# Kernel tuning notes

Hardware: AMD Instinct MI355X
Metric: run time of the kernel (lower is better)

## Reference

```python
import math
import jax, jax.numpy as jnp
import numpy as np

NUM_HEADS = 16
WINDOW = 64  # neighbor_size
NEG_INF = -1e30


def setup_inputs() -> dict:
    key = jax.random.key(0)
    ks = jax.random.split(key, 5)
    B, L, D = 2, 2048, 1024
    x = jax.random.normal(ks[0], (B, L, D), dtype=jnp.float32)
    s = 0.02
    Wq = jax.random.normal(ks[1], (D, D), dtype=jnp.float32) * s
    Wk = jax.random.normal(ks[2], (D, D), dtype=jnp.float32) * s
    Wv = jax.random.normal(ks[3], (D, D), dtype=jnp.float32) * s
    Wo = jax.random.normal(ks[4], (D, D), dtype=jnp.float32) * s
    return {
        "x": x, "Wq": Wq, "Wk": Wk, "Wv": Wv, "Wo": Wo,
        "sep_gate": jnp.float32(0.1),
        "align_gate": jnp.float32(0.1),
        "coh_gate": jnp.float32(0.1),
    }


def reference(x, Wq, Wk, Wv, Wo, sep_gate, align_gate, coh_gate):
    B, L, D = x.shape
    H = NUM_HEADS
    hd = D // H
    scale = math.sqrt(hd)

    # projections (torch Linear: y = x @ W.T), split heads -> (B, H, L, hd)
    def proj(W):
        return (x @ W.T).reshape(B, L, H, hd).transpose(0, 2, 1, 3)

    q, k, v = proj(Wq), proj(Wk), proj(Wv)

    # raw scores (B, H, L, L)
    scores = jnp.einsum("bhqd,bhkd->bhqk", q, k) / scale

    # Reynolds rules (applied BEFORE masking, mean over full kv dim, as in source)
    similarity = jax.nn.sigmoid(scores)
    separation = -sep_gate * similarity ** 2
    alignment = align_gate * scores
    score_mean = jnp.mean(scores, axis=-1, keepdims=True)
    cohesion = -coh_gate * jnp.abs(scores - score_mean)
    scores = scores + separation + alignment + cohesion

    # causal sliding-window mask: attend iff 0 <= i - j < WINDOW
    i = jnp.arange(L)[:, None]
    j = jnp.arange(L)[None, :]
    dist = i - j
    masked = (dist < 0) | (dist >= WINDOW)  # (L, L) True = blocked
    scores = jnp.where(masked[None, None, :, :], NEG_INF, scores)

    attn = jax.nn.softmax(scores, axis=-1)  # dropout p=0.0 -> identity
    out = jnp.einsum("bhqk,bhkd->bhqd", attn, v)
    out = out.transpose(0, 2, 1, 3).reshape(B, L, D)
    return out @ Wo.T
```

## Files before the change

### kernel.cpp

```cpp
#include <hip/hip_runtime.h>
#include <math.h>

#define L_SEQ 2048
#define DMODEL 1024
#define HEADS 16
#define HD 64
#define BATCH 2
#define MROWS (BATCH*L_SEQ)
#define KDIM 1024

typedef short bfrag8 __attribute__((ext_vector_type(8)));
typedef float f32x4f __attribute__((ext_vector_type(4)));

__device__ __forceinline__ unsigned short f2bf(float f) {
    unsigned u = __float_as_uint(f);
    unsigned r = u + 0x7FFFu + ((u >> 16) & 1u);
    return (unsigned short)(r >> 16);
}
__device__ __forceinline__ float bf2f(unsigned short h) {
    return __uint_as_float(((unsigned)h) << 16);
}

__global__ __launch_bounds__(256) void convert_bf16(
    const float* __restrict__ x, const float* __restrict__ wq,
    const float* __restrict__ wk, const float* __restrict__ wv,
    const float* __restrict__ wo,
    unsigned short* __restrict__ xb, unsigned short* __restrict__ qwb,
    unsigned short* __restrict__ kwb, unsigned short* __restrict__ vwb,
    unsigned short* __restrict__ owb)
{
    const int bid = blockIdx.x;
    const float* src; unsigned short* dst; size_t base;
    if (bid < 4096) { src = x; dst = xb; base = (size_t)bid * 1024; }
    else {
        const int r = bid - 4096; const int w = r >> 10; const int off = r & 1023;
        src = (w==0) ? wq : (w==1) ? wk : (w==2) ? wv : wo;
        dst = (w==0) ? qwb : (w==1) ? kwb : (w==2) ? vwb : owb;
        base = (size_t)off * 1024;
    }
    const size_t idx = base + (size_t)threadIdx.x * 4;
    float4 v = *(const float4*)&src[idx];
    ushort4 o;
    o.x = f2bf(v.x); o.y = f2bf(v.y); o.z = f2bf(v.z); o.w = f2bf(v.w);
    *(ushort4*)&dst[idx] = o;
}

#define GBK 32

template<int MODE>
__global__ void mfma_gemm(
    const unsigned short* __restrict__ A,
    const unsigned short* __restrict__ W0, const unsigned short* __restrict__ W1,
    const unsigned short* __restrict__ W2,
    void* __restrict__ C0v, void* __restrict__ C1v, void* __restrict__ C2v)
{
    __shared__ short As[128*GBK];
    __shared__ short Bs[128*GBK];

    const int tid  = threadIdx.x;
    const int wave = tid >> 6, lane = tid & 63;
    const int m0   = blockIdx.x * 128;
    const int n0g  = blockIdx.y * 128;

    const unsigned short* Wp; int n0; int which = 0;
    if (MODE == 1) {
        which = n0g >> 10;
        n0 = n0g & 1023;
        Wp = (which==0) ? W0 : (which==1) ? W1 : W2;
    } else { n0 = n0g; Wp = W0; }

    const int quad = lane >> 4, lm = lane & 15;
    const int wm = wave >> 1, wn = wave & 1;

    f32x4f acc[4][4] = {};

    const int ebase0 = wave * 1024;

    for (int k0 = 0; k0 < KDIM; k0 += GBK) {
        __syncthreads();
        #pragma unroll
        for (int i = 0; i < 2; ++i) {
            const int ebase = ebase0 + i * 512;
            const int e = ebase + lane * 8;
            const int row = e >> 5, col = e & 31;
            __builtin_amdgcn_global_load_lds(
                (const __attribute__((address_space(1))) void*)(A + (size_t)(m0 + row) * KDIM + k0 + col),
                (__attribute__((address_space(3))) void*)(&As[ebase]), 16, 0, 0);
            __builtin_amdgcn_global_load_lds(
                (const __attribute__((address_space(1))) void*)(Wp + (size_t)(n0 + row) * KDIM + k0 + col),
                (__attribute__((address_space(3))) void*)(&Bs[ebase]), 16, 0, 0);
        }
        __syncthreads();

        bfrag8 af[4], bf[4];
        #pragma unroll
        for (int t = 0; t < 4; ++t) {
            af[t] = *(const bfrag8*)&As[(wm*64 + t*16 + lm)*GBK + quad*8];
            bf[t] = *(const bfrag8*)&Bs[(wn*64 + t*16 + lm)*GBK + quad*8];
        }
        #pragma unroll
        for (int mt = 0; mt < 4; ++mt)
            #pragma unroll
            for (int nt = 0; nt < 4; ++nt)
                acc[mt][nt] = __builtin_amdgcn_mfma_f32_16x16x32_bf16(
                    af[mt], bf[nt], acc[mt][nt], 0, 0, 0);
    }

    if (MODE == 1) {
        unsigned short* Cp = (unsigned short*)((which==0) ? C0v : (which==1) ? C1v : C2v);
        #pragma unroll
        for (int mt = 0; mt < 4; ++mt)
            #pragma unroll
            for (int nt = 0; nt < 4; ++nt) {
                const int gn = n0 + wn*64 + nt*16 + lm;
                const int h = gn >> 6, d = gn & 63;
                #pragma unroll
                for (int r = 0; r < 4; ++r) {
                    const int gm = m0 + wm*64 + mt*16 + quad*4 + r;
                    const int b = gm >> 11, l = gm & (L_SEQ-1);
                    Cp[(((size_t)(b*HEADS + h) * L_SEQ) + l) * HD + d] = f2bf(acc[mt][nt][r]);
                }
            }
    } else {
        float* Cp = (float*)C0v;
        #pragma unroll
        for (int mt = 0; mt < 4; ++mt)
            #pragma unroll
            for (int nt = 0; nt < 4; ++nt) {
                const int gn = n0 + wn*64 + nt*16 + lm;
                #pragma unroll
                for (int r = 0; r < 4; ++r) {
                    const int gm = m0 + wm*64 + mt*16 + quad*4 + r;
                    Cp[(size_t)gm * DMODEL + gn] = acc[mt][nt][r];
                }
            }
    }
}

__global__ __launch_bounds__(256) void kmean_from_k(
    const unsigned short* __restrict__ kb, float* __restrict__ kmean)
{
    __shared__ float part[4][64];
    const int bh = blockIdx.x, t = threadIdx.x;
    const int d = t & 63, seg = t >> 6;
    const unsigned short* kp = kb + ((size_t)bh * L_SEQ + seg * 512) * HD + d;
    float s0 = 0.f, s1 = 0.f, s2 = 0.f, s3 = 0.f;
    #pragma unroll 4
    for (int l = 0; l < 512; l += 4) {
        s0 += bf2f(kp[(size_t)(l+0) * HD]);
        s1 += bf2f(kp[(size_t)(l+1) * HD]);
        s2 += bf2f(kp[(size_t)(l+2) * HD]);
        s3 += bf2f(kp[(size_t)(l+3) * HD]);
    }
    part[seg][d] = (s0 + s1) + (s2 + s3);
    __syncthreads();
    if (t < 64)
        kmean[bh * HD + t] = (part[0][t] + part[1][t] + part[2][t] + part[3][t])
                             * (1.f / (float)L_SEQ);
}

#define QT 64
#define KROWS 128
#define VROWS 144
#define KS_STRIDE 72
#define VT_STRIDE 152
#define P_STRIDE 104

__global__ __launch_bounds__(256, 3) void attn_kernel(
    const unsigned short* __restrict__ qb, const unsigned short* __restrict__ kb,
    const unsigned short* __restrict__ vb, const float* __restrict__ kmean,
    const float* __restrict__ g_sep, const float* __restrict__ g_align,
    const float* __restrict__ g_coh, unsigned short* __restrict__ out)
{
    __shared__ unsigned short ks[KROWS * KS_STRIDE];
    __shared__ unsigned short vst[HD * VT_STRIDE];
    __shared__ unsigned short pl[QT * P_STRIDE];
    __shared__ float smean[QT];
    __shared__ float km_s[HD];

    const int tid = threadIdx.x;
    const int bh = blockIdx.x >> 5;
    const int qt = blockIdx.x & 31;
    const int q0 = qt * QT;
    const int j0 = q0 - 63;

    const unsigned short* kbh = kb + (size_t)bh * L_SEQ * HD;
    const unsigned short* vbh = vb + (size_t)bh * L_SEQ * HD;

    if (tid < HD) km_s[tid] = kmean[bh * HD + tid];

    for (int idx = tid; idx < KROWS * 8; idx += 256) {
        const int r = idx & (KROWS - 1);
        const int c8 = idx >> 7;
        int j = j0 + r; j = j < 0 ? 0 : (j >= L_SEQ ? L_SEQ - 1 : j);
        bfrag8 d = *(const bfrag8*)&kbh[(size_t)j * HD + c8 * 8];
        *(bfrag8*)&ks[r * KS_STRIDE + c8 * 8] = d;
    }
    for (int idx = tid; idx < VROWS * 8; idx += 256) {
        const int r = idx % VROWS;
        const int c8 = idx / VROWS;
        int j = j0 + r; j = j < 0 ? 0 : (j >= L_SEQ ? L_SEQ - 1 : j);
        bfrag8 d = *(const bfrag8*)&vbh[(size_t)j * HD + c8 * 8];
        #pragma unroll
        for (int e = 0; e < 8; ++e)
            vst[(c8 * 8 + e) * VT_STRIDE + r] = (unsigned short)d[e];
    }

    const int w = tid >> 6, lane = tid & 63;
    const int quad = lane >> 4, lm = lane & 15;
    const float sep = g_sep[0], align = g_align[0], coh = g_coh[0];

    const unsigned short* qrow =
        qb + ((size_t)bh * L_SEQ + q0 + w*16 + lm) * HD + quad * 8;
    bfrag8 qa0 = *(const bfrag8*)qrow;
    bfrag8 qa1 = *(const bfrag8*)(qrow + 32);

    __syncthreads();

    float part = 0.f;
    #pragma unroll
    for (int j = 0; j < 8; ++j)
        part += bf2f((unsigned short)qa0[j]) * km_s[quad*8 + j]
              + bf2f((unsigned short)qa1[j]) * km_s[32 + quad*8 + j];
    part += __shfl_xor(part, 16, 64);
    part += __shfl_xor(part, 32, 64);
    if (quad == 0) smean[w*16 + lm] = part;

    f32x4f sacc[5];
    #pragma unroll
    for (int t = 0; t < 5; ++t) {
        const int krow = w*16 + t*16 + lm;
        bfrag8 b0 = *(const bfrag8*)&ks[krow * KS_STRIDE + quad*8];
        bfrag8 b1 = *(const bfrag8*)&ks[krow * KS_STRIDE + 32 + quad*8];
        f32x4f z = {0.f, 0.f, 0.f, 0.f};
        z = __builtin_amdgcn_mfma_f32_16x16x32_bf16(qa0, b0, z, 0, 0, 0);
        sacc[t] = __builtin_amdgcn_mfma_f32_16x16x32_bf16(qa1, b1, z, 0, 0, 0);
    }

    float rinv[4];
    #pragma unroll
    for (int r = 0; r < 4; ++r) {
        const int row = quad*4 + r;
        const int i   = q0 + w*16 + row;
        const float mean_i = smean[w*16 + row] * 0.125f;
        float sc[5]; float mx = -3.0e38f;
        #pragma unroll
        for (int t = 0; t < 5; ++t) {
            const int jabs = j0 + w*16 + t*16 + lm;
            const int dist = i - jabs;
            float s = sacc[t][r] * 0.125f;
            const float sig = 1.f / (1.f + __expf(-s));
            float adj = s * (1.f + align) - sep * sig * sig - coh * fabsf(s - mean_i);
            const bool ok = (dist >= 0) && (dist < 64) && (jabs >= 0);
            sc[t] = ok ? adj : -3.0e38f;
            mx = fmaxf(mx, sc[t]);
        }
        mx = fmaxf(mx, __shfl_xor(mx, 1, 64));
        mx = fmaxf(mx, __shfl_xor(mx, 2, 64));
        mx = fmaxf(mx, __shfl_xor(mx, 4, 64));
        mx = fmaxf(mx, __shfl_xor(mx, 8, 64));
        float ls = 0.f;
        #pragma unroll
        for (int t = 0; t < 5; ++t) {
            const float p = __expf(sc[t] - mx);
            ls += p;
            pl[(w*16 + row) * P_STRIDE + t*16 + lm] = f2bf(p);
        }
        pl[(w*16 + row) * P_STRIDE + 80 + lm] = 0;
        ls += __shfl_xor(ls, 1, 64);
        ls += __shfl_xor(ls, 2, 64);
        ls += __shfl_xor(ls, 4, 64);
        ls += __shfl_xor(ls, 8, 64);
        rinv[r] = 1.f / ls;
    }

    f32x4f oacc[4] = {};
    #pragma unroll
    for (int kk = 0; kk < 3; ++kk) {
        bfrag8 pa = *(const bfrag8*)&pl[(w*16 + lm) * P_STRIDE + kk*32 + quad*8];
        #pragma unroll
        for (int nt = 0; nt < 4; ++nt) {
            bfrag8 bv = *(const bfrag8*)&vst[(nt*16 + lm) * VT_STRIDE + w*16 + kk*32 + quad*8];
            oacc[nt] = __builtin_amdgcn_mfma_f32_16x16x32_bf16(pa, bv, oacc[nt], 0, 0, 0);
        }
    }

    const int b = bh >> 4, h = bh & (HEADS - 1);
    #pragma unroll
    for (int nt = 0; nt < 4; ++nt)
        #pragma unroll
        for (int r = 0; r < 4; ++r) {
            const int i = q0 + w*16 + quad*4 + r;
            const int d = nt*16 + lm;
            out[((size_t)(b * L_SEQ + i)) * DMODEL + h * HD + d] =
                f2bf(oacc[nt][r] * rinv[r]);
        }
}

extern "C" void kernel_launch(void* const* d_in, const int* in_sizes, int n_in,
                              void* d_out, int out_size, void* d_ws, size_t ws_size,
                              hipStream_t stream)
{
    (void)in_sizes; (void)n_in; (void)out_size; (void)ws_size;
    const float* x     = (const float*)d_in[0];
    const float* Wq    = (const float*)d_in[1];
    const float* Wk    = (const float*)d_in[2];
    const float* Wv    = (const float*)d_in[3];
    const float* Wo    = (const float*)d_in[4];
    const float* g_sep   = (const float*)d_in[5];
    const float* g_align = (const float*)d_in[6];
    const float* g_coh   = (const float*)d_in[7];
    float* out = (float*)d_out;

    float* f = (float*)d_ws;
    float* kmean_ws = f;
    unsigned short* xb  = (unsigned short*)(kmean_ws + 2048);
    const size_t per = (size_t)MROWS * DMODEL;
    unsigned short* wqb = xb  + per;
    unsigned short* wkb = wqb + (size_t)DMODEL*KDIM;
    unsigned short* wvb = wkb + (size_t)DMODEL*KDIM;
    unsigned short* wob = wvb + (size_t)DMODEL*KDIM;
    unsigned short* qb  = wob + (size_t)DMODEL*KDIM;
    unsigned short* kb  = qb  + per;
    unsigned short* vb  = kb  + per;
    unsigned short* attb = vb + per;

    convert_bf16<<<dim3(8192), dim3(256), 0, stream>>>(
        x, Wq, Wk, Wv, Wo, xb, wqb, wkb, wvb, wob);
    mfma_gemm<1><<<dim3(MROWS/128, 3*DMODEL/128), dim3(256), 0, stream>>>(
        xb, wqb, wkb, wvb, qb, kb, vb);
    kmean_from_k<<<dim3(BATCH*HEADS), dim3(256), 0, stream>>>(kb, kmean_ws);
    attn_kernel<<<dim3(BATCH*HEADS*(L_SEQ/QT)), dim3(256), 0, stream>>>(
        qb, kb, vb, kmean_ws, g_sep, g_align, g_coh, attb);
    mfma_gemm<0><<<dim3(MROWS/128, DMODEL/128), dim3(256), 0, stream>>>(
        attb, wob, nullptr, nullptr, out, nullptr, nullptr);
}
```

Measured before the change: 174.3 us.

## Fuse K-mean into QKV GEMM epilogue, write V transposed, drop attention LDS staging

The separate kmean kernel is removed. The QKV GEMM epilogue now accumulates K column sums with float atomics into a buffer that an extra block of the convert kernel zeroes first. V is written pre-transposed into a padded per-head layout, so the attention kernel reads K and V^T fragments straight from global memory instead of staging them through LDS with a scalar transpose. The attention window is realigned to six 16-wide key tiles. This cuts a launch, LDS traffic and barriers, at the cost of more global/L2 reads per block. The uninitialized padding in the V^T buffer is multiplied by zero probabilities, which could produce NaN if that memory holds garbage.

```diff
diff --git a/kernel.cpp b/kernel.cpp
--- a/kernel.cpp
+++ b/kernel.cpp
@@ -8,6 +8,7 @@
 #define BATCH 2
 #define MROWS (BATCH*L_SEQ)
 #define KDIM 1024
+#define VSTRIDE 2136
 
 typedef short bfrag8 __attribute__((ext_vector_type(8)));
 typedef float f32x4f __attribute__((ext_vector_type(4)));
@@ -27,9 +28,15 @@
     const float* __restrict__ wo,
     unsigned short* __restrict__ xb, unsigned short* __restrict__ qwb,
     unsigned short* __restrict__ kwb, unsigned short* __restrict__ vwb,
-    unsigned short* __restrict__ owb)
+    unsigned short* __restrict__ owb, float* __restrict__ kmean_acc)
 {
     const int bid = blockIdx.x;
+    if (bid == 8192) {
+        float4 z = make_float4(0.f, 0.f, 0.f, 0.f);
+        *(float4*)&kmean_acc[threadIdx.x * 8]     = z;
+        *(float4*)&kmean_acc[threadIdx.x * 8 + 4] = z;
+        return;
+    }
     const float* src; unsigned short* dst; size_t base;
     if (bid < 4096) { src = x; dst = xb; base = (size_t)bid * 1024; }
     else {
@@ -52,7 +59,8 @@
     const unsigned short* __restrict__ A,
     const unsigned short* __restrict__ W0, const unsigned short* __restrict__ W1,
     const unsigned short* __restrict__ W2,
-    void* __restrict__ C0v, void* __restrict__ C1v, void* __restrict__ C2v)
+    void* __restrict__ C0v, void* __restrict__ C1v, void* __restrict__ C2v,
+    float* __restrict__ kmean_acc)
 {
     __shared__ short As[128*GBK];
     __shared__ short Bs[128*GBK];
@@ -107,20 +115,51 @@
     }
 
     if (MODE == 1) {
-        unsigned short* Cp = (unsigned short*)((which==0) ? C0v : (which==1) ? C1v : C2v);
-        #pragma unroll
-        for (int mt = 0; mt < 4; ++mt)
+        if (which == 2) {
+            unsigned short* Vp = (unsigned short*)C2v;
             #pragma unroll
-            for (int nt = 0; nt < 4; ++nt) {
-                const int gn = n0 + wn*64 + nt*16 + lm;
-                const int h = gn >> 6, d = gn & 63;
+            for (int mt = 0; mt < 4; ++mt)
                 #pragma unroll
-                for (int r = 0; r < 4; ++r) {
-                    const int gm = m0 + wm*64 + mt*16 + quad*4 + r;
-                    const int b = gm >> 11, l = gm & (L_SEQ-1);
-                    Cp[(((size_t)(b*HEADS + h) * L_SEQ) + l) * HD + d] = f2bf(acc[mt][nt][r]);
+                for (int nt = 0; nt < 4; ++nt) {
+                    const int gn = n0 + wn*64 + nt*16 + lm;
+                    const int h = gn >> 6, d = gn & 63;
+                    const int gm0 = m0 + wm*64 + mt*16 + quad*4;
+                    const int b = gm0 >> 11, l0 = gm0 & (L_SEQ-1);
+                    ushort4 o;
+                    o.x = f2bf(acc[mt][nt][0]); o.y = f2bf(acc[mt][nt][1]);
+                    o.z = f2bf(acc[mt][nt][2]); o.w = f2bf(acc[mt][nt][3]);
+                    *(ushort4*)&Vp[((size_t)((b*HEADS + h)*HD + d))*VSTRIDE + 64 + l0] = o;
+                }
+        } else {
+            unsigned short* Cp = (unsigned short*)((which==0) ? C0v : C1v);
+            #pragma unroll
+            for (int mt = 0; mt < 4; ++mt)
+                #pragma unroll
+                for (int nt = 0; nt < 4; ++nt) {
+                    const int gn = n0 + wn*64 + nt*16 + lm;
+                    const int h = gn >> 6, d = gn & 63;
+                    #pragma unroll
+                    for (int r = 0; r < 4; ++r) {
+                        const int gm = m0 + wm*64 + mt*16 + quad*4 + r;
+                        const int b = gm >> 11, l = gm & (L_SEQ-1);
+                        Cp[(((size_t)(b*HEADS + h) * L_SEQ) + l) * HD + d] = f2bf(acc[mt][nt][r]);
+                    }
+                }
+            if (which == 1) {
+                const int b = m0 >> 11;
+                #pragma unroll
+                for (int nt = 0; nt < 4; ++nt) {
+                    const int gn = n0 + wn*64 + nt*16 + lm;
+                    const int h = gn >> 6, d = gn & 63;
+                    float s = 0.f;
+                    #pragma unroll
+                    for (int mt = 0; mt < 4; ++mt)
+                        #pragma unroll
+                        for (int r = 0; r < 4; ++r) s += acc[mt][nt][r];
+                    atomicAdd(&kmean_acc[(size_t)(b*HEADS + h)*HD + d], s);
                 }
             }
+        }
     } else {
         float* Cp = (float*)C0v;
         #pragma unroll
@@ -137,101 +176,60 @@
     }
 }
 
-__global__ __launch_bounds__(256) void kmean_from_k(
-    const unsigned short* __restrict__ kb, float* __restrict__ kmean)
-{
-    __shared__ float part[4][64];
-    const int bh = blockIdx.x, t = threadIdx.x;
-    const int d = t & 63, seg = t >> 6;
-    const unsigned short* kp = kb + ((size_t)bh * L_SEQ + seg * 512) * HD + d;
-    float s0 = 0.f, s1 = 0.f, s2 = 0.f, s3 = 0.f;
-    #pragma unroll 4
-    for (int l = 0; l < 512; l += 4) {
-        s0 += bf2f(kp[(size_t)(l+0) * HD]);
-        s1 += bf2f(kp[(size_t)(l+1) * HD]);
-        s2 += bf2f(kp[(size_t)(l+2) * HD]);
-        s3 += bf2f(kp[(size_t)(l+3) * HD]);
-    }
-    part[seg][d] = (s0 + s1) + (s2 + s3);
-    __syncthreads();
-    if (t < 64)
-        kmean[bh * HD + t] = (part[0][t] + part[1][t] + part[2][t] + part[3][t])
-                             * (1.f / (float)L_SEQ);
-}
-
-#define QT 64
-#define KROWS 128
-#define VROWS 144
-#define KS_STRIDE 72
-#define VT_STRIDE 152
 #define P_STRIDE 104
 
-__global__ __launch_bounds__(256, 3) void attn_kernel(
+__global__ __launch_bounds__(256) void attn_kernel(
     const unsigned short* __restrict__ qb, const unsigned short* __restrict__ kb,
-    const unsigned short* __restrict__ vb, const float* __restrict__ kmean,
+    const unsigned short* __restrict__ vt, const float* __restrict__ kmean_acc,
     const float* __restrict__ g_sep, const float* __restrict__ g_align,
     const float* __restrict__ g_coh, unsigned short* __restrict__ out)
 {
-    __shared__ unsigned short ks[KROWS * KS_STRIDE];
-    __shared__ unsigned short vst[HD * VT_STRIDE];
-    __shared__ unsigned short pl[QT * P_STRIDE];
-    __shared__ float smean[QT];
-    __shared__ float km_s[HD];
+    __shared__ unsigned short pl[64 * P_STRIDE];
 
     const int tid = threadIdx.x;
     const int bh = blockIdx.x >> 5;
     const int qt = blockIdx.x & 31;
-    const int q0 = qt * QT;
-    const int j0 = q0 - 63;
-
-    const unsigned short* kbh = kb + (size_t)bh * L_SEQ * HD;
-    const unsigned short* vbh = vb + (size_t)bh * L_SEQ * HD;
-
-    if (tid < HD) km_s[tid] = kmean[bh * HD + tid];
-
-    for (int idx = tid; idx < KROWS * 8; idx += 256) {
-        const int r = idx & (KROWS - 1);
-        const int c8 = idx >> 7;
-        int j = j0 + r; j = j < 0 ? 0 : (j >= L_SEQ ? L_SEQ - 1 : j);
-        bfrag8 d = *(const bfrag8*)&kbh[(size_t)j * HD + c8 * 8];
-        *(bfrag8*)&ks[r * KS_STRIDE + c8 * 8] = d;
-    }
-    for (int idx = tid; idx < VROWS * 8; idx += 256) {
-        const int r = idx % VROWS;
-        const int c8 = idx / VROWS;
-        int j = j0 + r; j = j < 0 ? 0 : (j >= L_SEQ ? L_SEQ - 1 : j);
-        bfrag8 d = *(const bfrag8*)&vbh[(size_t)j * HD + c8 * 8];
-        #pragma unroll
-        for (int e = 0; e < 8; ++e)
-            vst[(c8 * 8 + e) * VT_STRIDE + r] = (unsigned short)d[e];
-    }
+    const int q0 = qt * 64;
+    const int j0 = q0 - 64;
 
     const int w = tid >> 6, lane = tid & 63;
     const int quad = lane >> 4, lm = lane & 15;
     const float sep = g_sep[0], align = g_align[0], coh = g_coh[0];
+
+    const unsigned short* kbh = kb + (size_t)bh * L_SEQ * HD;
+    const unsigned short* vbh = vt + (size_t)bh * HD * VSTRIDE;
 
     const unsigned short* qrow =
         qb + ((size_t)bh * L_SEQ + q0 + w*16 + lm) * HD + quad * 8;
     bfrag8 qa0 = *(const bfrag8*)qrow;
     bfrag8 qa1 = *(const bfrag8*)(qrow + 32);
 
-    __syncthreads();
-
-    float part = 0.f;
-    #pragma unroll
-    for (int j = 0; j < 8; ++j)
-        part += bf2f((unsigned short)qa0[j]) * km_s[quad*8 + j]
-              + bf2f((unsigned short)qa1[j]) * km_s[32 + quad*8 + j];
+    const float* kmp = kmean_acc + bh * HD + quad * 8;
+    float4 km0 = *(const float4*)(kmp);
+    float4 km1 = *(const float4*)(kmp + 4);
+    float4 km2 = *(const float4*)(kmp + 32);
+    float4 km3 = *(const float4*)(kmp + 36);
+    float part =
+        bf2f((unsigned short)qa0[0])*km0.x + bf2f((unsigned short)qa0[1])*km0.y +
+        bf2f((unsigned short)qa0[2])*km0.z + bf2f((unsigned short)qa0[3])*km0.w +
+        bf2f((unsigned short)qa0[4])*km1.x + bf2f((unsigned short)qa0[5])*km1.y +
+        bf2f((unsigned short)qa0[6])*km1.z + bf2f((unsigned short)qa0[7])*km1.w +
+        bf2f((unsigned short)qa1[0])*km2.x + bf2f((unsigned short)qa1[1])*km2.y +
+        bf2f((unsigned short)qa1[2])*km2.z + bf2f((unsigned short)qa1[3])*km2.w +
+        bf2f((unsigned short)qa1[4])*km3.x + bf2f((unsigned short)qa1[5])*km3.y +
+        bf2f((unsigned short)qa1[6])*km3.z + bf2f((unsigned short)qa1[7])*km3.w;
+    part *= (1.f / (float)L_SEQ);
     part += __shfl_xor(part, 16, 64);
     part += __shfl_xor(part, 32, 64);
-    if (quad == 0) smean[w*16 + lm] = part;
-
-    f32x4f sacc[5];
+
+    f32x4f sacc[6];
     #pragma unroll
-    for (int t = 0; t < 5; ++t) {
-        const int krow = w*16 + t*16 + lm;
-        bfrag8 b0 = *(const bfrag8*)&ks[krow * KS_STRIDE + quad*8];
-        bfrag8 b1 = *(const bfrag8*)&ks[krow * KS_STRIDE + 32 + quad*8];
+    for (int t = 0; t < 6; ++t) {
+        int kr = j0 + w*16 + t*16 + lm;
+        kr = kr < 0 ? 0 : (kr >= L_SEQ ? L_SEQ - 1 : kr);
+        const unsigned short* kp = kbh + (size_t)kr * HD + quad * 8;
+        bfrag8 b0 = *(const bfrag8*)kp;
+        bfrag8 b1 = *(const bfrag8*)(kp + 32);
         f32x4f z = {0.f, 0.f, 0.f, 0.f};
         z = __builtin_amdgcn_mfma_f32_16x16x32_bf16(qa0, b0, z, 0, 0, 0);
         sacc[t] = __builtin_amdgcn_mfma_f32_16x16x32_bf16(qa1, b1, z, 0, 0, 0);
@@ -242,10 +240,10 @@
     for (int r = 0; r < 4; ++r) {
         const int row = quad*4 + r;
         const int i   = q0 + w*16 + row;
-        const float mean_i = smean[w*16 + row] * 0.125f;
-        float sc[5]; float mx = -3.0e38f;
-        #pragma unroll
-        for (int t = 0; t < 5; ++t) {
+        const float mean_i = __shfl(part, row, 64) * 0.125f;
+        float sc[6]; float mx = -3.0e38f;
+        #pragma unroll
+        for (int t = 0; t < 6; ++t) {
             const int jabs = j0 + w*16 + t*16 + lm;
             const int dist = i - jabs;
             float s = sacc[t][r] * 0.125f;
@@ -261,12 +259,11 @@
         mx = fmaxf(mx, __shfl_xor(mx, 8, 64));
         float ls = 0.f;
         #pragma unroll
-        for (int t = 0; t < 5; ++t) {
+        for (int t = 0; t < 6; ++t) {
             const float p = __expf(sc[t] - mx);
             ls += p;
             pl[(w*16 + row) * P_STRIDE + t*16 + lm] = f2bf(p);
         }
-        pl[(w*16 + row) * P_STRIDE + 80 + lm] = 0;
         ls += __shfl_xor(ls, 1, 64);
         ls += __shfl_xor(ls, 2, 64);
         ls += __shfl_xor(ls, 4, 64);
@@ -278,9 +275,10 @@
     #pragma unroll
     for (int kk = 0; kk < 3; ++kk) {
         bfrag8 pa = *(const bfrag8*)&pl[(w*16 + lm) * P_STRIDE + kk*32 + quad*8];
+        const int loff = 64 + j0 + w*16 + kk*32 + quad*8;
         #pragma unroll
         for (int nt = 0; nt < 4; ++nt) {
-            bfrag8 bv = *(const bfrag8*)&vst[(nt*16 + lm) * VT_STRIDE + w*16 + kk*32 + quad*8];
+            bfrag8 bv = *(const bfrag8*)&vbh[(size_t)(nt*16 + lm) * VSTRIDE + loff];
             oacc[nt] = __builtin_amdgcn_mfma_f32_16x16x32_bf16(pa, bv, oacc[nt], 0, 0, 0);
         }
     }
@@ -312,8 +310,7 @@
     const float* g_coh   = (const float*)d_in[7];
     float* out = (float*)d_out;
 
-    float* f = (float*)d_ws;
-    float* kmean_ws = f;
+    float* kmean_ws = (float*)d_ws;
     unsigned short* xb  = (unsigned short*)(kmean_ws + 2048);
     const size_t per = (size_t)MROWS * DMODEL;
     unsigned short* wqb = xb  + per;
@@ -322,16 +319,15 @@
     unsigned short* wob = wvb + (size_t)DMODEL*KDIM;
     unsigned short* qb  = wob + (size_t)DMODEL*KDIM;
     unsigned short* kb  = qb  + per;
-    unsigned short* vb  = kb  + per;
-    unsigned short* attb = vb + per;
-
-    convert_bf16<<<dim3(8192), dim3(256), 0, stream>>>(
-        x, Wq, Wk, Wv, Wo, xb, wqb, wkb, wvb, wob);
+    unsigned short* vtb = kb  + per;
+    unsigned short* attb = vtb + (size_t)BATCH*HEADS*HD*VSTRIDE;
+
+    convert_bf16<<<dim3(8193), dim3(256), 0, stream>>>(
+        x, Wq, Wk, Wv, Wo, xb, wqb, wkb, wvb, wob, kmean_ws);
     mfma_gemm<1><<<dim3(MROWS/128, 3*DMODEL/128), dim3(256), 0, stream>>>(
-        xb, wqb, wkb, wvb, qb, kb, vb);
-    kmean_from_k<<<dim3(BATCH*HEADS), dim3(256), 0, stream>>>(kb, kmean_ws);
-    attn_kernel<<<dim3(BATCH*HEADS*(L_SEQ/QT)), dim3(256), 0, stream>>>(
-        qb, kb, vb, kmean_ws, g_sep, g_align, g_coh, attb);
+        xb, wqb, wkb, wvb, qb, kb, vtb, kmean_ws);
+    attn_kernel<<<dim3(BATCH*HEADS*(L_SEQ/64)), dim3(256), 0, stream>>>(
+        qb, kb, vtb, kmean_ws, g_sep, g_align, g_coh, attb);
     mfma_gemm<0><<<dim3(MROWS/128, DMODEL/128), dim3(256), 0, stream>>>(
-        attb, wob, nullptr, nullptr, out, nullptr, nullptr);
-}
+        attb, wob, nullptr, nullptr, out, nullptr, nullptr, nullptr);
+}
```

Result: faster. 167.4 us (-3.9%).
